# Kernel tuning notes

Hardware: AMD Instinct MI355X
Metric: run time of the kernel (lower is better)

## Reference

```python
import jax, jax.numpy as jnp
import numpy as np

D = 1024        # d_hidden
DE = 512        # d_expert (routed)
E = 8           # n_routed_experts
TOP_K = 2
DS = DE * 2     # shared expert width = d_expert * n_shared_experts


def setup_inputs() -> dict:
    key = jax.random.key(0)
    ks = jax.random.split(key, 8)
    s = 1.0 / np.sqrt(D)
    return {
        "x": jax.random.normal(ks[0], (2, 1024, D), dtype=jnp.float32),
        "W_g": jax.random.normal(ks[1], (D, E), dtype=jnp.float32) * s,
        "Wg_e": jax.random.normal(ks[2], (E, D, DE), dtype=jnp.float32) * s,
        "Wu_e": jax.random.normal(ks[3], (E, D, DE), dtype=jnp.float32) * s,
        "Wd_e": jax.random.normal(ks[4], (E, DE, D), dtype=jnp.float32) * (1.0 / np.sqrt(DE)),
        "Wg_s": jax.random.normal(ks[5], (D, DS), dtype=jnp.float32) * s,
        "Wu_s": jax.random.normal(ks[6], (D, DS), dtype=jnp.float32) * s,
        "Wd_s": jax.random.normal(ks[7], (DS, D), dtype=jnp.float32) * (1.0 / np.sqrt(DS)),
    }


def _moe(x, W_g, Wg_e, Wu_e, Wd_e, Wg_s, Wu_s, Wd_s):
    B, T, Dm = x.shape
    N = B * T
    xf = x.reshape(N, Dm)

    # shared expert (SwiGLU)
    shared = (jax.nn.silu(xf @ Wg_s) * (xf @ Wu_s)) @ Wd_s  # [N, D]

    # gating: softmax then top-k (set membership identical to torch sorted=False)
    probs = jax.nn.softmax(xf @ W_g, axis=-1)               # [N, E]
    topk_vals, topk_ids = jax.lax.top_k(probs, TOP_K)       # [N, K]

    # combine weights c[n, e] = sum of topk_vals where routed to expert e
    # (equivalent to the original gather -> weighted scatter_add combine)
    c = jnp.zeros((N, E), dtype=x.dtype)
    c = c.at[jnp.arange(N)[:, None], topk_ids].add(topk_vals)

    # dense per-expert SwiGLU, weighted-combined (same math as gather/scatter loop)
    gate = jax.nn.silu(jnp.einsum('nd,edh->neh', xf, Wg_e))
    up = jnp.einsum('nd,edh->neh', xf, Wu_e)
    routed = jnp.einsum('neh,ne,ehd->nd', gate * up, c, Wd_e)  # [N, D]

    return (shared + routed).reshape(B, T, Dm)


def reference(x, W_g, Wg_e, Wu_e, Wd_e, Wg_s, Wu_s, Wd_s):
    return _moe(x, W_g, Wg_e, Wu_e, Wd_e, Wg_s, Wu_s, Wd_s)
```

## Files before the change

### kernel.cpp

```cpp
#include <hip/hip_runtime.h>
#include <hip/hip_bf16.h>

#define NTOK 2048
#define DIM  1024
#define DEXP 512
#define NEXP 8
#define DSH  1024
#define KH   5120
#define MAXROWS 5120
#define PACKBLOCKS 3840

typedef __hip_bfloat16 bf16;
typedef __attribute__((ext_vector_type(8))) short bf16x8;
typedef __attribute__((ext_vector_type(4))) float floatx4;

__device__ __forceinline__ void gl_lds16(const bf16* g, bf16* l) {
    __builtin_amdgcn_global_load_lds(
        (const __attribute__((address_space(1))) void*)g,
        (__attribute__((address_space(3))) void*)l, 16, 0, 0);
}

__device__ __forceinline__ float b2f(short s) {
    union { float f; unsigned u; } v;
    v.u = ((unsigned)(unsigned short)s) << 16;
    return v.f;
}

struct B4 { bf16 a, b, c, d; };

__global__ __launch_bounds__(128) void pack_gate(
        const float* __restrict__ Wg_s, const float* __restrict__ Wu_s,
        const float* __restrict__ Wg_e, const float* __restrict__ Wu_e,
        const float* __restrict__ Wd_s, const float* __restrict__ Wd_e,
        const float* __restrict__ x, const float* __restrict__ Wg,
        bf16* __restrict__ Bg, bf16* __restrict__ Bu, bf16* __restrict__ Bd,
        bf16* __restrict__ Xb, int2* __restrict__ te, float2* __restrict__ tp) {
    int b = blockIdx.x;
    const int tid = threadIdx.x;
    if (b < PACKBLOCKS) {
        __shared__ unsigned lt[64][35];
        const float* src; bf16* dst; int C; long dstStride, dstBase; int tilesX;
        if (b < 256)        { src = Wg_s; dst = Bg; C = 1024; dstStride = 1024; dstBase = 0; tilesX = 16; }
        else if (b < 1280)  { int z = (b - 256) >> 7; b = (b - 256) & 127;
                              src = Wg_e + (long)z * DIM * DEXP; dst = Bg; C = 512;
                              dstStride = 1024; dstBase = (long)(DSH + z * DEXP) * 1024; tilesX = 8; }
        else if (b < 1536)  { b -= 1280; src = Wu_s; dst = Bu; C = 1024; dstStride = 1024; dstBase = 0; tilesX = 16; }
        else if (b < 2560)  { int z = (b - 1536) >> 7; b = (b - 1536) & 127;
                              src = Wu_e + (long)z * DIM * DEXP; dst = Bu; C = 512;
                              dstStride = 1024; dstBase = (long)(DSH + z * DEXP) * 1024; tilesX = 8; }
        else if (b < 2816)  { b -= 2560; src = Wd_s; dst = Bd; C = 1024; dstStride = KH; dstBase = 0; tilesX = 16; }
        else                { int z = (b - 2816) >> 7; b = (b - 2816) & 127;
                              src = Wd_e + (long)z * DEXP * DIM; dst = Bd; C = 1024;
                              dstStride = KH; dstBase = DSH + (long)z * DEXP; tilesX = 16; }
        const int tileX = b & (tilesX - 1), tileY = b / tilesX;
        const int c0 = tileX * 64, r0 = tileY * 64;

        const int lrow = tid >> 4, lch = tid & 15;
#pragma unroll
        for (int i = 0; i < 8; i++) {
            int row = lrow + i * 8;
            float4 v = *(const float4*)(src + (long)(r0 + row) * C + c0 + lch * 4);
            union { bf16 h[2]; unsigned u; } p0, p1;
            p0.h[0] = __float2bfloat16(v.x); p0.h[1] = __float2bfloat16(v.y);
            p1.h[0] = __float2bfloat16(v.z); p1.h[1] = __float2bfloat16(v.w);
            lt[row][lch * 2]     = p0.u;
            lt[row][lch * 2 + 1] = p1.u;
        }
        __syncthreads();
        const int kc = tid & 7;
#pragma unroll
        for (int i = 0; i < 4; i++) {
            int h = (tid >> 3) + i * 16;
            union { unsigned short s[8]; bf16x8 v8; } o;
#pragma unroll
            for (int j = 0; j < 8; j++)
                o.s[j] = ((const unsigned short*)lt[kc * 8 + j])[h];
            *(bf16x8*)(dst + dstBase + (long)(c0 + h) * dstStride + r0 + kc * 8) = o.v8;
        }
    } else {
        int t = (b - PACKBLOCKS) * 2 + (tid >> 6);
        int lane = tid & 63;
        const float* xr = x + (long)t * DIM;
        bf16* xo = Xb + (long)t * DIM;
        float acc[NEXP] = {0.f, 0.f, 0.f, 0.f, 0.f, 0.f, 0.f, 0.f};
#pragma unroll
        for (int i = 0; i < 4; i++) {
            int d = lane * 4 + i * 256;
            float4 xv = *(const float4*)(xr + d);
            B4 o{__float2bfloat16(xv.x), __float2bfloat16(xv.y),
                 __float2bfloat16(xv.z), __float2bfloat16(xv.w)};
            *(B4*)(xo + d) = o;
#pragma unroll
            for (int j = 0; j < 4; j++) {
                float xs = (j == 0) ? xv.x : (j == 1) ? xv.y : (j == 2) ? xv.z : xv.w;
                float4 w0 = *(const float4*)(Wg + (d + j) * NEXP);
                float4 w1 = *(const float4*)(Wg + (d + j) * NEXP + 4);
                acc[0] += xs * w0.x; acc[1] += xs * w0.y; acc[2] += xs * w0.z; acc[3] += xs * w0.w;
                acc[4] += xs * w1.x; acc[5] += xs * w1.y; acc[6] += xs * w1.z; acc[7] += xs * w1.w;
            }
        }
#pragma unroll
        for (int e = 0; e < NEXP; e++)
#pragma unroll
            for (int off = 32; off; off >>= 1)
                acc[e] += __shfl_xor(acc[e], off);
        if (lane == 0) {
            float m = acc[0];
#pragma unroll
            for (int e = 1; e < NEXP; e++) m = fmaxf(m, acc[e]);
            float p[NEXP], s = 0.f;
#pragma unroll
            for (int e = 0; e < NEXP; e++) { p[e] = expf(acc[e] - m); s += p[e]; }
            float inv = 1.f / s;
#pragma unroll
            for (int e = 0; e < NEXP; e++) p[e] *= inv;
            int i1 = 0;
#pragma unroll
            for (int e = 1; e < NEXP; e++) if (p[e] > p[i1]) i1 = e;
            int i2 = (i1 == 0) ? 1 : 0;
#pragma unroll
            for (int e = 0; e < NEXP; e++) if (e != i1 && p[e] > p[i2]) i2 = e;
            te[t] = make_int2(i1, i2);
            tp[t] = make_float2(p[i1], p[i2]);
        }
    }
}

__global__ __launch_bounds__(512) void assign_kernel(const int2* __restrict__ te,
                                                     const float2* __restrict__ tp,
                                                     int* __restrict__ counts,
                                                     int* __restrict__ offs,
                                                     int* __restrict__ tok_list,
                                                     float* __restrict__ cw,
                                                     int* __restrict__ s1a,
                                                     int* __restrict__ s2a) {
    __shared__ int cnt[NEXP];
    const int e = threadIdx.x >> 6;
    const int lane = threadIdx.x & 63;
    int base = 0;
    for (int t0 = 0; t0 < NTOK; t0 += 64) {
        int t = t0 + lane;
        int2 ee = te[t];
        bool m1 = (ee.x == e), m2 = (ee.y == e);
        bool mt = m1 || m2;
        unsigned long long mask = __ballot(mt);
        int pre = __popcll(mask & ((1ull << lane) - 1ull));
        if (mt) {
            int slot = base + pre;
            tok_list[e * NTOK + slot] = t;
            float2 pp = tp[t];
            cw[e * NTOK + slot] = m1 ? pp.x : pp.y;
            if (m1) s1a[t] = slot; else s2a[t] = slot;
        }
        base += __popcll(mask);
    }
    if (lane == 0) cnt[e] = base;
    __syncthreads();
    if (threadIdx.x == 0) {
        int o = 0;
#pragma unroll
        for (int i = 0; i < NEXP; i++) {
            counts[i] = cnt[i];
            offs[i] = o;
            o += (cnt[i] + 127) & ~127;
        }
    }
}

__global__ __launch_bounds__(256) void gu_all(const bf16* __restrict__ X,
                                              const bf16* __restrict__ Bg,
                                              const bf16* __restrict__ Bu,
                                              const int* __restrict__ counts,
                                              const int* __restrict__ offs,
                                              const int* __restrict__ tok_list,
                                              const float* __restrict__ cw,
                                              bf16* __restrict__ Hs,
                                              bf16* __restrict__ He) {
    __shared__ __align__(16) bf16 sA[3][128 * 32];
    __shared__ __align__(16) bf16 sBg[3][64 * 32];
    __shared__ __align__(16) bf16 sBu[3][64 * 32];

    const int b = blockIdx.x;
    const bool routed = b < 1024;
    int e = 0, m, c;
    if (routed) {
        e = b >> 7; m = (b >> 3) & 15; c = b & 7;
        if (m * 128 >= counts[e]) return;
    } else {
        int bs = b - 1024; m = bs >> 4; c = bs & 15;
    }
    const int so = routed ? offs[e] : 0;
    const int colB0 = routed ? (DSH + e * DEXP + c * 64) : c * 64;

    const int tid = threadIdx.x;
    const int wave = tid >> 6, lane = tid & 63;
    const int wr = wave >> 1, wc = wave & 1;
    const int q = lane >> 4, l15 = lane & 15;
    const int koff = (q ^ ((l15 >> 1) & 3)) * 8;

    const int r0 = tid >> 2, c4 = tid & 3;
    const int r1 = r0 + 64;
    const int c4s = c4 ^ ((r0 >> 1) & 3);
    long aRow0, aRow1;
    if (routed) {
        const int* tl = tok_list + e * NTOK + m * 128;
        aRow0 = (long)tl[r0] * DIM;
        aRow1 = (long)tl[r1] * DIM;
    } else {
        aRow0 = (long)(m * 128 + r0) * DIM;
        aRow1 = (long)(m * 128 + r1) * DIM;
    }
    const long bRow = (long)(colB0 + r0) * DIM;

    floatx4 accG[4][2], accU[4][2];
    const floatx4 z4 = {0.f, 0.f, 0.f, 0.f};
#pragma unroll
    for (int i = 0; i < 4; i++)
#pragma unroll
        for (int j = 0; j < 2; j++) { accG[i][j] = z4; accU[i][j] = z4; }

    auto stage = [&](int bb, int k0) {
        gl_lds16(X + aRow0 + k0 + c4s * 8, &sA[bb][wave * 512]);
        gl_lds16(X + aRow1 + k0 + c4s * 8, &sA[bb][2048 + wave * 512]);
        gl_lds16(Bg + bRow + k0 + c4s * 8, &sBg[bb][wave * 512]);
        gl_lds16(Bu + bRow + k0 + c4s * 8, &sBu[bb][wave * 512]);
    };
    auto compute = [&](int bb) {
        bf16x8 af[4], bgv[2], buv[2];
#pragma unroll
        for (int rt = 0; rt < 4; rt++)
            af[rt] = *(const bf16x8*)(&sA[bb][(wr * 64 + rt * 16 + l15) * 32 + koff]);
#pragma unroll
        for (int ct = 0; ct < 2; ct++) {
            int cb = (wc * 32 + ct * 16 + l15) * 32 + koff;
            bgv[ct] = *(const bf16x8*)(&sBg[bb][cb]);
            buv[ct] = *(const bf16x8*)(&sBu[bb][cb]);
        }
#pragma unroll
        for (int rt = 0; rt < 4; rt++)
#pragma unroll
            for (int ct = 0; ct < 2; ct++) {
                accG[rt][ct] = __builtin_amdgcn_mfma_f32_16x16x32_bf16(af[rt], bgv[ct], accG[rt][ct], 0, 0, 0);
                accU[rt][ct] = __builtin_amdgcn_mfma_f32_16x16x32_bf16(af[rt], buv[ct], accU[rt][ct], 0, 0, 0);
            }
    };

    const int NS = DIM / 32;
    stage(0, 0);
    stage(1, 32);
    int bb = 0;
    for (int ks = 0; ks < NS; ks++) {
        if (ks + 2 < NS) stage((bb + 2) % 3, (ks + 2) * 32);
        if (ks + 2 < NS)      asm volatile("s_waitcnt vmcnt(8)" ::: "memory");
        else if (ks + 1 < NS) asm volatile("s_waitcnt vmcnt(4)" ::: "memory");
        else                  asm volatile("s_waitcnt vmcnt(0)" ::: "memory");
        __builtin_amdgcn_s_barrier();
        asm volatile("" ::: "memory");
        compute(bb);
        asm volatile("" ::: "memory");
        __builtin_amdgcn_s_barrier();
        bb = (bb + 1) % 3;
    }

    float wv[4][4];
#pragma unroll
    for (int rt = 0; rt < 4; rt++)
#pragma unroll
        for (int r = 0; r < 4; r++) {
            int srow = wr * 64 + rt * 16 + q * 4 + r;
            wv[rt][r] = routed ? cw[e * NTOK + m * 128 + srow] : 1.0f;
        }
#pragma unroll
    for (int rt = 0; rt < 4; rt++)
#pragma unroll
        for (int ct = 0; ct < 2; ct++)
#pragma unroll
            for (int r = 0; r < 4; r++) {
                int srow = wr * 64 + rt * 16 + q * 4 + r;
                int colLoc = c * 64 + wc * 32 + ct * 16 + l15;
                float g = accG[rt][ct][r];
                float u = accU[rt][ct][r];
                float h = (g / (1.f + __expf(-g))) * u * wv[rt][r];
                if (routed)
                    He[(long)(so + m * 128 + srow) * DEXP + colLoc] = __float2bfloat16(h);
                else
                    Hs[(long)(m * 128 + srow) * DSH + colLoc] = __float2bfloat16(h);
            }
}

__global__ __launch_bounds__(256) void down_all(const bf16* __restrict__ Hs,
                                                const bf16* __restrict__ He,
                                                const bf16* __restrict__ Bd,
                                                const int* __restrict__ counts,
                                                const int* __restrict__ offs,
                                                bf16* __restrict__ Ys,
                                                bf16* __restrict__ Ye) {
    __shared__ __align__(16) bf16 sA[3][128 * 32];
    __shared__ __align__(16) bf16 sB[3][64 * 32];

    const int b = blockIdx.x;
    const bool routed = b < 2048;
    int e = 0, m, cc;
    if (routed) {
        e = b >> 8; m = (b >> 4) & 15; cc = b & 15;
        if (m * 128 >= counts[e]) return;
    } else {
        int bs = b - 2048; m = bs >> 4; cc = bs & 15;
    }
    const int so = routed ? offs[e] : 0;
    const bf16* A = routed ? He + (long)so * DEXP : Hs;
    bf16* Y = routed ? Ye + (long)so * DIM : Ys;
    const int astr = routed ? DEXP : DSH;
    const int ksteps = routed ? (DEXP / 32) : (DSH / 32);
    const int kg0 = routed ? (DSH + e * DEXP) : 0;

    const int tid = threadIdx.x;
    const int wave = tid >> 6, lane = tid & 63;
    const int wr = wave >> 1, wc = wave & 1;
    const int q = lane >> 4, l15 = lane & 15;
    const int koff = (q ^ ((l15 >> 1) & 3)) * 8;

    const int r0 = tid >> 2, c4 = tid & 3;
    const int r1 = r0 + 64;
    const int c4s = c4 ^ ((r0 >> 1) & 3);
    const long aRow0 = (long)(m * 128 + r0) * astr;
    const long aRow1 = (long)(m * 128 + r1) * astr;
    const long bRow = (long)(cc * 64 + r0) * KH + kg0;

    floatx4 acc[4][2];
    const floatx4 z4 = {0.f, 0.f, 0.f, 0.f};
#pragma unroll
    for (int i = 0; i < 4; i++)
#pragma unroll
        for (int j = 0; j < 2; j++) acc[i][j] = z4;

    auto stage = [&](int bb, int k0) {
        gl_lds16(A + aRow0 + k0 + c4s * 8, &sA[bb][wave * 512]);
        gl_lds16(A + aRow1 + k0 + c4s * 8, &sA[bb][2048 + wave * 512]);
        gl_lds16(Bd + bRow + k0 + c4s * 8, &sB[bb][wave * 512]);
    };
    auto compute = [&](int bb) {
        bf16x8 af[4], bb2[2];
#pragma unroll
        for (int rt = 0; rt < 4; rt++)
            af[rt] = *(const bf16x8*)(&sA[bb][(wr * 64 + rt * 16 + l15) * 32 + koff]);
#pragma unroll
        for (int ct = 0; ct < 2; ct++)
            bb2[ct] = *(const bf16x8*)(&sB[bb][(wc * 32 + ct * 16 + l15) * 32 + koff]);
#pragma unroll
        for (int rt = 0; rt < 4; rt++)
#pragma unroll
            for (int ct = 0; ct < 2; ct++)
                acc[rt][ct] = __builtin_amdgcn_mfma_f32_16x16x32_bf16(af[rt], bb2[ct], acc[rt][ct], 0, 0, 0);
    };

    stage(0, 0);
    stage(1, 32);
    int bb = 0;
    for (int ks = 0; ks < ksteps; ks++) {
        if (ks + 2 < ksteps) stage((bb + 2) % 3, (ks + 2) * 32);
        if (ks + 2 < ksteps)      asm volatile("s_waitcnt vmcnt(6)" ::: "memory");
        else if (ks + 1 < ksteps) asm volatile("s_waitcnt vmcnt(3)" ::: "memory");
        else                      asm volatile("s_waitcnt vmcnt(0)" ::: "memory");
        __builtin_amdgcn_s_barrier();
        asm volatile("" ::: "memory");
        compute(bb);
        asm volatile("" ::: "memory");
        __builtin_amdgcn_s_barrier();
        bb = (bb + 1) % 3;
    }

#pragma unroll
    for (int rt = 0; rt < 4; rt++)
#pragma unroll
        for (int ct = 0; ct < 2; ct++)
#pragma unroll
            for (int r = 0; r < 4; r++) {
                int srow = wr * 64 + rt * 16 + q * 4 + r;
                int mc = cc * 64 + wc * 32 + ct * 16 + l15;
                Y[(long)(m * 128 + srow) * DIM + mc] = __float2bfloat16(acc[rt][ct][r]);
            }
}

__global__ __launch_bounds__(256) void combine_kernel(const bf16* __restrict__ Ys,
                                                      const bf16* __restrict__ Ye,
                                                      const int2* __restrict__ te,
                                                      const int* __restrict__ s1a,
                                                      const int* __restrict__ s2a,
                                                      const int* __restrict__ offs,
                                                      float* __restrict__ out) {
    int idx = blockIdx.x * 256 + threadIdx.x;
    int t = idx >> 7;
    int d = (idx & 127) * 8;
    int2 ee = te[t];
    long r1 = (long)(offs[ee.x] + s1a[t]);
    long r2 = (long)(offs[ee.y] + s2a[t]);
    bf16x8 a = *(const bf16x8*)(Ys + (long)t * DIM + d);
    bf16x8 p = *(const bf16x8*)(Ye + r1 * DIM + d);
    bf16x8 r = *(const bf16x8*)(Ye + r2 * DIM + d);
    float* o = out + (long)t * DIM + d;
#pragma unroll
    for (int i = 0; i < 8; i++)
        o[i] = b2f(a[i]) + b2f(p[i]) + b2f(r[i]);
}

extern "C" void kernel_launch(void* const* d_in, const int* in_sizes, int n_in,
                              void* d_out, int out_size, void* d_ws, size_t ws_size,
                              hipStream_t stream) {
    const float* x    = (const float*)d_in[0];
    const float* W_g  = (const float*)d_in[1];
    const float* Wg_e = (const float*)d_in[2];
    const float* Wu_e = (const float*)d_in[3];
    const float* Wd_e = (const float*)d_in[4];
    const float* Wg_s = (const float*)d_in[5];
    const float* Wu_s = (const float*)d_in[6];
    const float* Wd_s = (const float*)d_in[7];
    float* out = (float*)d_out;

    bf16* Xb = (bf16*)d_ws;
    bf16* Bg = Xb + (size_t)NTOK * DIM;
    bf16* Bu = Bg + (size_t)KH * DIM;
    bf16* Bd = Bu + (size_t)KH * DIM;
    bf16* Hs = Bd + (size_t)DIM * KH;
    bf16* He = Hs + (size_t)NTOK * DSH;
    bf16* Ys = He + (size_t)MAXROWS * DEXP;
    bf16* Ye = Ys + (size_t)NTOK * DIM;
    int*  counts   = (int*)(Ye + (size_t)MAXROWS * DIM);
    int*  offs     = counts + NEXP;
    int*  tok_list = offs + NEXP;
    float* cw      = (float*)(tok_list + NEXP * NTOK);
    int*  s1a      = (int*)(cw + NEXP * NTOK);
    int*  s2a      = s1a + NTOK;
    int2* te       = (int2*)(s2a + NTOK);
    float2* tp     = (float2*)(te + NTOK);

    hipMemsetAsync(tok_list, 0,
                   sizeof(int) * NEXP * NTOK + sizeof(float) * NEXP * NTOK, stream);
    pack_gate<<<PACKBLOCKS + NTOK / 2, 128, 0, stream>>>(
        Wg_s, Wu_s, Wg_e, Wu_e, Wd_s, Wd_e, x, W_g, Bg, Bu, Bd, Xb, te, tp);
    assign_kernel<<<1, 512, 0, stream>>>(te, tp, counts, offs, tok_list, cw, s1a, s2a);
    gu_all<<<1280, 256, 0, stream>>>(Xb, Bg, Bu, counts, offs, tok_list, cw, Hs, He);
    down_all<<<2304, 256, 0, stream>>>(Hs, He, Bd, counts, offs, Ys, Ye);
    combine_kernel<<<NTOK * DIM / 8 / 256, 256, 0, stream>>>(Ys, Ye, te, s1a, s2a, offs, out);
}
```

Measured before the change: 209.7 us.

## Fuse combine into down GEMM epilogue with float atomic scatter-add

Removes the separate combine kernel and the bf16 Ys/Ye intermediate buffers. The down-projection epilogue now atomically adds its fp32 accumulators straight into the zeroed output, using tok_list to map routed rows back to tokens. Padding rows in tok_list/cw are zeroed inside assign_kernel rather than by a large memset, and the output is memset instead. This saves a kernel launch and the intermediate round trip, but costs three global float atomics per output element, and the summation order now varies between runs.

```diff
diff --git a/kernel.cpp b/kernel.cpp
--- a/kernel.cpp
+++ b/kernel.cpp
@@ -18,12 +18,6 @@
     __builtin_amdgcn_global_load_lds(
         (const __attribute__((address_space(1))) void*)g,
         (__attribute__((address_space(3))) void*)l, 16, 0, 0);
-}
-
-__device__ __forceinline__ float b2f(short s) {
-    union { float f; unsigned u; } v;
-    v.u = ((unsigned)(unsigned short)s) << 16;
-    return v.f;
 }
 
 struct B4 { bf16 a, b, c, d; };
@@ -131,9 +125,7 @@
                                                      int* __restrict__ counts,
                                                      int* __restrict__ offs,
                                                      int* __restrict__ tok_list,
-                                                     float* __restrict__ cw,
-                                                     int* __restrict__ s1a,
-                                                     int* __restrict__ s2a) {
+                                                     float* __restrict__ cw) {
     __shared__ int cnt[NEXP];
     const int e = threadIdx.x >> 6;
     const int lane = threadIdx.x & 63;
@@ -150,9 +142,13 @@
             tok_list[e * NTOK + slot] = t;
             float2 pp = tp[t];
             cw[e * NTOK + slot] = m1 ? pp.x : pp.y;
-            if (m1) s1a[t] = slot; else s2a[t] = slot;
         }
         base += __popcll(mask);
+    }
+    int rounded = (base + 127) & ~127;
+    for (int s = base + lane; s < rounded; s += 64) {
+        tok_list[e * NTOK + s] = 0;
+        cw[e * NTOK + s] = 0.f;
     }
     if (lane == 0) cnt[e] = base;
     __syncthreads();
@@ -293,8 +289,8 @@
                                                 const bf16* __restrict__ Bd,
                                                 const int* __restrict__ counts,
                                                 const int* __restrict__ offs,
-                                                bf16* __restrict__ Ys,
-                                                bf16* __restrict__ Ye) {
+                                                const int* __restrict__ tok_list,
+                                                float* __restrict__ out) {
     __shared__ __align__(16) bf16 sA[3][128 * 32];
     __shared__ __align__(16) bf16 sB[3][64 * 32];
 
@@ -309,7 +305,6 @@
     }
     const int so = routed ? offs[e] : 0;
     const bf16* A = routed ? He + (long)so * DEXP : Hs;
-    bf16* Y = routed ? Ye + (long)so * DIM : Ys;
     const int astr = routed ? DEXP : DSH;
     const int ksteps = routed ? (DEXP / 32) : (DSH / 32);
     const int kg0 = routed ? (DSH + e * DEXP) : 0;
@@ -371,37 +366,21 @@
     }
 
 #pragma unroll
-    for (int rt = 0; rt < 4; rt++)
-#pragma unroll
-        for (int ct = 0; ct < 2; ct++)
-#pragma unroll
-            for (int r = 0; r < 4; r++) {
-                int srow = wr * 64 + rt * 16 + q * 4 + r;
-                int mc = cc * 64 + wc * 32 + ct * 16 + l15;
-                Y[(long)(m * 128 + srow) * DIM + mc] = __float2bfloat16(acc[rt][ct][r]);
-            }
-}
-
-__global__ __launch_bounds__(256) void combine_kernel(const bf16* __restrict__ Ys,
-                                                      const bf16* __restrict__ Ye,
-                                                      const int2* __restrict__ te,
-                                                      const int* __restrict__ s1a,
-                                                      const int* __restrict__ s2a,
-                                                      const int* __restrict__ offs,
-                                                      float* __restrict__ out) {
-    int idx = blockIdx.x * 256 + threadIdx.x;
-    int t = idx >> 7;
-    int d = (idx & 127) * 8;
-    int2 ee = te[t];
-    long r1 = (long)(offs[ee.x] + s1a[t]);
-    long r2 = (long)(offs[ee.y] + s2a[t]);
-    bf16x8 a = *(const bf16x8*)(Ys + (long)t * DIM + d);
-    bf16x8 p = *(const bf16x8*)(Ye + r1 * DIM + d);
-    bf16x8 r = *(const bf16x8*)(Ye + r2 * DIM + d);
-    float* o = out + (long)t * DIM + d;
-#pragma unroll
-    for (int i = 0; i < 8; i++)
-        o[i] = b2f(a[i]) + b2f(p[i]) + b2f(r[i]);
+    for (int rt = 0; rt < 4; rt++) {
+        int tk[4];
+#pragma unroll
+        for (int r = 0; r < 4; r++) {
+            int srow = wr * 64 + rt * 16 + q * 4 + r;
+            tk[r] = routed ? tok_list[e * NTOK + m * 128 + srow] : (m * 128 + srow);
+        }
+#pragma unroll
+        for (int ct = 0; ct < 2; ct++) {
+            int mc = cc * 64 + wc * 32 + ct * 16 + l15;
+#pragma unroll
+            for (int r = 0; r < 4; r++)
+                atomicAdd(&out[(long)tk[r] * DIM + mc], acc[rt][ct][r]);
+        }
+    }
 }
 
 extern "C" void kernel_launch(void* const* d_in, const int* in_sizes, int n_in,
@@ -423,23 +402,17 @@
     bf16* Bd = Bu + (size_t)KH * DIM;
     bf16* Hs = Bd + (size_t)DIM * KH;
     bf16* He = Hs + (size_t)NTOK * DSH;
-    bf16* Ys = He + (size_t)MAXROWS * DEXP;
-    bf16* Ye = Ys + (size_t)NTOK * DIM;
-    int*  counts   = (int*)(Ye + (size_t)MAXROWS * DIM);
+    int*  counts   = (int*)(He + (size_t)MAXROWS * DEXP);
     int*  offs     = counts + NEXP;
     int*  tok_list = offs + NEXP;
     float* cw      = (float*)(tok_list + NEXP * NTOK);
-    int*  s1a      = (int*)(cw + NEXP * NTOK);
-    int*  s2a      = s1a + NTOK;
-    int2* te       = (int2*)(s2a + NTOK);
+    int2* te       = (int2*)(cw + NEXP * NTOK);
     float2* tp     = (float2*)(te + NTOK);
 
-    hipMemsetAsync(tok_list, 0,
-                   sizeof(int) * NEXP * NTOK + sizeof(float) * NEXP * NTOK, stream);
+    hipMemsetAsync(out, 0, (size_t)NTOK * DIM * sizeof(float), stream);
     pack_gate<<<PACKBLOCKS + NTOK / 2, 128, 0, stream>>>(
         Wg_s, Wu_s, Wg_e, Wu_e, Wd_s, Wd_e, x, W_g, Bg, Bu, Bd, Xb, te, tp);
-    assign_kernel<<<1, 512, 0, stream>>>(te, tp, counts, offs, tok_list, cw, s1a, s2a);
+    assign_kernel<<<1, 512, 0, stream>>>(te, tp, counts, offs, tok_list, cw);
     gu_all<<<1280, 256, 0, stream>>>(Xb, Bg, Bu, counts, offs, tok_list, cw, Hs, He);
-    down_all<<<2304, 256, 0, stream>>>(Hs, He, Bd, counts, offs, Ys, Ye);
-    combine_kernel<<<NTOK * DIM / 8 / 256, 256, 0, stream>>>(Ys, Ye, te, s1a, s2a, offs, out);
-}
+    down_all<<<2304, 256, 0, stream>>>(Hs, He, Bd, counts, offs, tok_list, out);
+}
```

After: 261.5 us. 1.25x slower.

## Move down-proj weight packing into gate/up kernel and drop memset

Applied to the files above, without the earlier changes.

The fp32-to-bf16 transpose-pack of the shared and routed down-projection weights moves out of the first pack kernel into extra blocks appended to the gate/up GEMM grid. Those blocks run alongside the GEMM tiles, so packing overlaps with compute and the first kernel gets shorter. The hipMemsetAsync of the token list and combine weights is replaced by zeroing only the padded tail slots of each expert inside the assign kernel. The cost is a larger gu_all grid with heterogeneous blocks, which may contend with the GEMM for bandwidth and scheduling.

```diff
diff --git a/kernel.cpp b/kernel.cpp
--- a/kernel.cpp
+++ b/kernel.cpp
@@ -8,7 +8,7 @@
 #define DSH  1024
 #define KH   5120
 #define MAXROWS 5120
-#define PACKBLOCKS 3840
+#define PACKBLOCKS 2560
 
 typedef __hip_bfloat16 bf16;
 typedef __attribute__((ext_vector_type(8))) short bf16x8;
@@ -31,27 +31,22 @@
 __global__ __launch_bounds__(128) void pack_gate(
         const float* __restrict__ Wg_s, const float* __restrict__ Wu_s,
         const float* __restrict__ Wg_e, const float* __restrict__ Wu_e,
-        const float* __restrict__ Wd_s, const float* __restrict__ Wd_e,
         const float* __restrict__ x, const float* __restrict__ Wg,
-        bf16* __restrict__ Bg, bf16* __restrict__ Bu, bf16* __restrict__ Bd,
+        bf16* __restrict__ Bg, bf16* __restrict__ Bu,
         bf16* __restrict__ Xb, int2* __restrict__ te, float2* __restrict__ tp) {
     int b = blockIdx.x;
     const int tid = threadIdx.x;
     if (b < PACKBLOCKS) {
         __shared__ unsigned lt[64][35];
-        const float* src; bf16* dst; int C; long dstStride, dstBase; int tilesX;
-        if (b < 256)        { src = Wg_s; dst = Bg; C = 1024; dstStride = 1024; dstBase = 0; tilesX = 16; }
+        const float* src; bf16* dst; int C; long dstBase; int tilesX;
+        if (b < 256)        { src = Wg_s; dst = Bg; C = 1024; dstBase = 0; tilesX = 16; }
         else if (b < 1280)  { int z = (b - 256) >> 7; b = (b - 256) & 127;
                               src = Wg_e + (long)z * DIM * DEXP; dst = Bg; C = 512;
-                              dstStride = 1024; dstBase = (long)(DSH + z * DEXP) * 1024; tilesX = 8; }
-        else if (b < 1536)  { b -= 1280; src = Wu_s; dst = Bu; C = 1024; dstStride = 1024; dstBase = 0; tilesX = 16; }
-        else if (b < 2560)  { int z = (b - 1536) >> 7; b = (b - 1536) & 127;
+                              dstBase = (long)(DSH + z * DEXP) * 1024; tilesX = 8; }
+        else if (b < 1536)  { b -= 1280; src = Wu_s; dst = Bu; C = 1024; dstBase = 0; tilesX = 16; }
+        else                { int z = (b - 1536) >> 7; b = (b - 1536) & 127;
                               src = Wu_e + (long)z * DIM * DEXP; dst = Bu; C = 512;
-                              dstStride = 1024; dstBase = (long)(DSH + z * DEXP) * 1024; tilesX = 8; }
-        else if (b < 2816)  { b -= 2560; src = Wd_s; dst = Bd; C = 1024; dstStride = KH; dstBase = 0; tilesX = 16; }
-        else                { int z = (b - 2816) >> 7; b = (b - 2816) & 127;
-                              src = Wd_e + (long)z * DEXP * DIM; dst = Bd; C = 1024;
-                              dstStride = KH; dstBase = DSH + (long)z * DEXP; tilesX = 16; }
+                              dstBase = (long)(DSH + z * DEXP) * 1024; tilesX = 8; }
         const int tileX = b & (tilesX - 1), tileY = b / tilesX;
         const int c0 = tileX * 64, r0 = tileY * 64;
 
@@ -75,7 +70,7 @@
 #pragma unroll
             for (int j = 0; j < 8; j++)
                 o.s[j] = ((const unsigned short*)lt[kc * 8 + j])[h];
-            *(bf16x8*)(dst + dstBase + (long)(c0 + h) * dstStride + r0 + kc * 8) = o.v8;
+            *(bf16x8*)(dst + dstBase + (long)(c0 + h) * 1024 + r0 + kc * 8) = o.v8;
         }
     } else {
         int t = (b - PACKBLOCKS) * 2 + (tid >> 6);
@@ -154,6 +149,11 @@
         }
         base += __popcll(mask);
     }
+    int rounded = (base + 127) & ~127;
+    for (int s = base + lane; s < rounded; s += 64) {
+        tok_list[e * NTOK + s] = 0;
+        cw[e * NTOK + s] = 0.f;
+    }
     if (lane == 0) cnt[e] = base;
     __syncthreads();
     if (threadIdx.x == 0) {
@@ -174,6 +174,9 @@
                                               const int* __restrict__ offs,
                                               const int* __restrict__ tok_list,
                                               const float* __restrict__ cw,
+                                              const float* __restrict__ Wd_s,
+                                              const float* __restrict__ Wd_e,
+                                              bf16* __restrict__ Bd,
                                               bf16* __restrict__ Hs,
                                               bf16* __restrict__ He) {
     __shared__ __align__(16) bf16 sA[3][128 * 32];
@@ -181,6 +184,47 @@
     __shared__ __align__(16) bf16 sBu[3][64 * 32];
 
     const int b = blockIdx.x;
+
+    if (b >= 1280) {
+        unsigned* lt = (unsigned*)&sA[0][0];
+        int pb = b - 1280;
+        const float* src; long dstBase; int tileX, tileY;
+        if (pb < 256) {
+            src = Wd_s; dstBase = 0;
+            tileX = pb & 15; tileY = pb >> 4;
+        } else {
+            int q = pb - 256; int z = q >> 7; q &= 127;
+            src = Wd_e + (long)z * DEXP * DIM;
+            dstBase = DSH + (long)z * DEXP;
+            tileX = q & 15; tileY = q >> 4;
+        }
+        const int c0 = tileX * 64, r0 = tileY * 64;
+        const int tid = threadIdx.x;
+        const int lrow = tid >> 4, lch = tid & 15;
+#pragma unroll
+        for (int i = 0; i < 4; i++) {
+            int row = lrow + i * 16;
+            float4 v = *(const float4*)(src + (long)(r0 + row) * DIM + c0 + lch * 4);
+            union { bf16 h[2]; unsigned u; } p0, p1;
+            p0.h[0] = __float2bfloat16(v.x); p0.h[1] = __float2bfloat16(v.y);
+            p1.h[0] = __float2bfloat16(v.z); p1.h[1] = __float2bfloat16(v.w);
+            lt[row * 35 + lch * 2]     = p0.u;
+            lt[row * 35 + lch * 2 + 1] = p1.u;
+        }
+        __syncthreads();
+        const int kc = tid & 7;
+#pragma unroll
+        for (int i = 0; i < 2; i++) {
+            int h = (tid >> 3) + i * 32;
+            union { unsigned short s[8]; bf16x8 v8; } o;
+#pragma unroll
+            for (int j = 0; j < 8; j++)
+                o.s[j] = ((const unsigned short*)(lt + (kc * 8 + j) * 35))[h];
+            *(bf16x8*)(Bd + (long)(c0 + h) * KH + dstBase + r0 + kc * 8) = o.v8;
+        }
+        return;
+    }
+
     const bool routed = b < 1024;
     int e = 0, m, c;
     if (routed) {
@@ -434,12 +478,11 @@
     int2* te       = (int2*)(s2a + NTOK);
     float2* tp     = (float2*)(te + NTOK);
 
-    hipMemsetAsync(tok_list, 0,
-                   sizeof(int) * NEXP * NTOK + sizeof(float) * NEXP * NTOK, stream);
     pack_gate<<<PACKBLOCKS + NTOK / 2, 128, 0, stream>>>(
-        Wg_s, Wu_s, Wg_e, Wu_e, Wd_s, Wd_e, x, W_g, Bg, Bu, Bd, Xb, te, tp);
+        Wg_s, Wu_s, Wg_e, Wu_e, x, W_g, Bg, Bu, Xb, te, tp);
     assign_kernel<<<1, 512, 0, stream>>>(te, tp, counts, offs, tok_list, cw, s1a, s2a);
-    gu_all<<<1280, 256, 0, stream>>>(Xb, Bg, Bu, counts, offs, tok_list, cw, Hs, He);
+    gu_all<<<2560, 256, 0, stream>>>(Xb, Bg, Bu, counts, offs, tok_list, cw,
+                                     Wd_s, Wd_e, Bd, Hs, He);
     down_all<<<2304, 256, 0, stream>>>(Hs, He, Bd, counts, offs, Ys, Ye);
     combine_kernel<<<NTOK * DIM / 8 / 256, 256, 0, stream>>>(Ys, Ye, te, s1a, s2a, offs, out);
 }
```

New measurement: 201.4 us. -4.0%, faster.
